# Kernel optimization log

Measured on AMD Instinct MI355X. Metric: run time of the kernel, lower is better.

Reference implementation:

```python
import jax, jax.numpy as jnp
import numpy as np

EPS = 1e-8
N, E, T, HH, HE, HD = 20000, 320000, 4, 64, 16, 128


def _merge(a):
    # 'm d t -> (m t) d'
    m, d, t = a.shape
    return a.transpose(0, 2, 1).reshape(m * t, d)


def _sep(a, t):
    # '(m t) d -> m d t'
    mt, d = a.shape
    return a.reshape(mt // t, t, d).transpose(0, 2, 1)


def _mlp2(x, w1, b1, w2, b2, last_act):
    y = jax.nn.silu(x @ w1 + b1)
    y = y @ w2 + b2
    return jax.nn.silu(y) if last_act else y


def setup_inputs() -> dict:
    key = jax.random.key(0)
    ks = jax.random.split(key, 16)

    def lin(k, i, o):
        return jax.random.normal(k, (i, o), jnp.float32) / np.sqrt(i)

    in_edge = HH * 2 + 1 + HE  # 145
    return {
        "x": jax.random.normal(ks[0], (N, 3, T), jnp.float32),
        "h": jax.random.normal(ks[1], (N, HH, T), jnp.float32),
        "edge_index": jax.random.randint(ks[2], (2, E), 0, N),
        "edge_attr": jax.random.normal(ks[3], (E, HE, T), jnp.float32),
        "batch": jnp.zeros((N,), jnp.int64),
        "edge_w1": lin(ks[4], in_edge, HD), "edge_b1": jnp.zeros((HD,), jnp.float32),
        "edge_w2": lin(ks[5], HD, HD), "edge_b2": jnp.zeros((HD,), jnp.float32),
        "coord_w1": lin(ks[6], HD, HD), "coord_b1": jnp.zeros((HD,), jnp.float32),
        "coord_w2": lin(ks[7], HD, 1), "coord_b2": jnp.zeros((1,), jnp.float32),
        "node_w1": lin(ks[8], HH + HD, HD), "node_b1": jnp.zeros((HD,), jnp.float32),
        "node_w2": lin(ks[9], HD, HH), "node_b2": jnp.zeros((HH,), jnp.float32),
    }


def reference(x, h, edge_index, edge_attr, batch,
              edge_w1, edge_b1, edge_w2, edge_b2,
              coord_w1, coord_b1, coord_w2, coord_b2,
              node_w1, node_b1, node_w2, node_b2):
    row, col = edge_index[0], edge_index[1]
    t = x.shape[-1]
    n = x.shape[0]

    x_ij = x[row] - x[col]                                  # [E,3,T]
    x_ij_norm2 = (x_ij ** 2).sum(axis=1, keepdims=True)     # [E,1,T]

    m_in = jnp.concatenate((h[row], h[col], x_ij_norm2, edge_attr), axis=1)  # [E,2Hh+1+He,T]
    m_ij = _mlp2(_merge(m_in), edge_w1, edge_b1, edge_w2, edge_b2, True)     # [ET,HD]

    m_i = jax.ops.segment_sum(_sep(m_ij, t), row, num_segments=n)           # [N,HD,T]

    h_cat = jnp.concatenate((_merge(h), _merge(m_i)), axis=-1)               # [NT,Hh+HD]
    h_new = _sep(_mlp2(h_cat, node_w1, node_b1, node_w2, node_b2, False), t) # [N,Hh,T]

    coord_m_ij = _mlp2(m_ij, coord_w1, coord_b1, coord_w2, coord_b2, False)  # [ET,1]
    coord_m_ij = coord_m_ij / (jnp.sqrt(_merge(x_ij_norm2) + EPS) + 1.0)

    agg = jax.ops.segment_sum(_sep(coord_m_ij, t) * x_ij, row, num_segments=n)  # [N,3,T]
    cnt = jax.ops.segment_sum(jnp.ones((row.shape[0],), x.dtype), row, num_segments=n)
    x_new = x + agg / jnp.maximum(cnt, 1.0)[:, None, None]
    return (x_new, h_new)
```

## Files before the change

kernel.cpp:

```cpp
#include <hip/hip_runtime.h>
#include <hip/hip_bf16.h>
#include <math.h>

#define T 4
#define HH 64
#define HE 16
#define HD 128
#define EPSF 1e-8f

#define TE 16
#define ROWS 64
#define LDA 168
#define TN 16
#define LDAN 200

using frag8 = __attribute__((ext_vector_type(8))) short;
using f32x4 = __attribute__((ext_vector_type(4))) float;

__device__ __forceinline__ float silu_f(float v) {
    return v * __builtin_amdgcn_rcpf(1.f + __expf(-v));
}

__device__ __forceinline__ unsigned short f2b(float f) {
    __hip_bfloat16 h = __float2bfloat16(f);
    union { __hip_bfloat16 h; unsigned short u; } v; v.h = h;
    return v.u;
}
__device__ __forceinline__ unsigned pk2(float a, float b) {
    __hip_bfloat162 h2 = __float22bfloat162_rn(make_float2(a, b));
    union { __hip_bfloat162 h; unsigned u; } v; v.h = h2;
    return v.u;
}
__device__ __forceinline__ float b2f(unsigned u16) {
    union { unsigned u; float f; } v; v.u = u16 << 16; return v.f;
}
__device__ __forceinline__ void lds_fence() {
    asm volatile("s_waitcnt lgkmcnt(0)" ::: "memory");
}

__global__ void prep_weights(const float* __restrict__ w1, const float* __restrict__ w2,
                             const float* __restrict__ cw1, const float* __restrict__ nw1,
                             const float* __restrict__ nw2, unsigned short* __restrict__ wb)
{
    int i = blockIdx.x * 256 + threadIdx.x;
    if (i < 20480) {
        int n = i / 160, k = i - n * 160;
        float v;
        if (k < 128)      v = w1[k * 128 + n];
        else if (k < 144) v = w1[(129 + (k - 128)) * 128 + n];
        else if (k == 144) v = w1[128 * 128 + n];
        else              v = 0.f;
        wb[i] = f2b(v);
    } else if (i < 36864) {
        int j = i - 20480; int n = j >> 7, k = j & 127;
        wb[i] = f2b(w2[k * 128 + n]);
    } else if (i < 53248) {
        int j = i - 36864; int n = j >> 7, k = j & 127;
        wb[i] = f2b(cw1[k * 128 + n]);
    } else if (i < 77824) {
        int j = i - 53248; int n = j / 192, k = j - n * 192;
        wb[i] = f2b(nw1[k * 128 + n]);
    } else if (i < 86016) {
        int j = i - 77824; int n = j >> 7, k = j & 127;
        wb[i] = f2b(nw2[k * 64 + n]);
    }
}

__global__ void prep_h(const float* __restrict__ h, unsigned short* __restrict__ hb, int N)
{
    int i = blockIdx.x * 256 + threadIdx.x;
    if (i < N * 64) {
        int n = i >> 6, d = i & 63;
        float4 v = *(const float4*)(h + (size_t)i * 4);
        size_t base = (size_t)n * 256 + d;
        hb[base + 0]   = f2b(v.x);
        hb[base + 64]  = f2b(v.y);
        hb[base + 128] = f2b(v.z);
        hb[base + 192] = f2b(v.w);
    }
}

__global__ void hist_kernel(const int* __restrict__ ei, int* __restrict__ deg, int E) {
    int e = blockIdx.x * 256 + threadIdx.x;
    if (e < E) atomicAdd(&deg[ei[e]], 1);
}

__global__ __launch_bounds__(1024)
void scan_kernel(const int* __restrict__ deg, int* __restrict__ start, int N) {
    __shared__ int part[1024];
    int tid = threadIdx.x;
    int chunk = (N + 1023) >> 10;
    int b0 = tid * chunk;
    int s = 0;
    for (int i = 0; i < chunk; ++i) { int idx = b0 + i; if (idx < N) s += deg[idx]; }
    part[tid] = s;
    __syncthreads();
    for (int off = 1; off < 1024; off <<= 1) {
        int v = (tid >= off) ? part[tid - off] : 0;
        __syncthreads();
        part[tid] += v;
        __syncthreads();
    }
    int prefix = (tid > 0) ? part[tid - 1] : 0;
    for (int i = 0; i < chunk; ++i) {
        int idx = b0 + i;
        if (idx < N) { start[idx] = prefix; prefix += deg[idx]; }
    }
    if (tid == 1023) start[N] = part[1023];
}

__global__ void scatter_kernel(const int* __restrict__ ei, const int* __restrict__ start,
                               int* __restrict__ cursor, int* __restrict__ list, int E) {
    int e = blockIdx.x * 256 + threadIdx.x;
    if (e < E) {
        int r = ei[e];
        int p = atomicAdd(&cursor[r], 1);
        list[start[r] + p] = e;
    }
}

__global__ __launch_bounds__(256, 7)
void edge_kernel(const float* __restrict__ x, const unsigned short* __restrict__ hb,
                 const int* __restrict__ ei, const float* __restrict__ ea,
                 const int* __restrict__ list,
                 const unsigned short* __restrict__ w1b,
                 const unsigned short* __restrict__ w2b,
                 const unsigned short* __restrict__ cw1b,
                 const float* __restrict__ b1, const float* __restrict__ b2,
                 const float* __restrict__ cb1, const float* __restrict__ cb2,
                 const float* __restrict__ cw2,
                 float* __restrict__ m_i,
                 float* __restrict__ agg,
                 int N, int E)
{
    __shared__ unsigned short sA[ROWS * LDA];
    __shared__ float sXij[TE * 12];
    __shared__ float sNorm[ROWS];
    __shared__ int   sNode[TE];
    __shared__ int   sPN[2];
    __shared__ float sCoord[ROWS];

    const int tid  = threadIdx.x;
    const int e0   = blockIdx.x * TE;
    const int lane = tid & 63;
    const int wid  = tid >> 6;
    const int eb   = wid * 4;

    if (tid < ROWS) sCoord[tid] = 0.f;
    if (tid == 0) {
        sPN[0] = (e0 > 0)      ? ei[list[e0 - 1]]  : -2;
        sPN[1] = (e0 + TE < E) ? ei[list[e0 + TE]] : -2;
    }

    int node8 = 0;
    {
        int le = lane >> 1, half = lane & 1;
        int p = e0 + eb + le;
        if (lane < 8 && p < E) {
            int eid = list[p];
            node8 = ei[half ? (E + eid) : eid];
            if (half == 0) sNode[eb + le] = node8;
        }
    }
    if (lane < 48) {
        int le = lane / 12, i = lane - le * 12;
        int p = e0 + eb + le;
        float d = 0.f;
        if (p < E) {
            int eid = list[p];
            d = x[ei[eid] * 12 + i] - x[ei[E + eid] * 12 + i];
        }
        sXij[(eb + le) * 12 + i] = d;
    }
    {
        int half = lane >> 5, t = (lane >> 3) & 3, chunk = lane & 7;
        #pragma unroll
        for (int le = 0; le < 4; ++le) {
            int p = e0 + eb + le;
            if (p < E) {
                int nid = __shfl(node8, le * 2 + half);
                uint4 v = *((const uint4*)hb + (size_t)nid * 32 + t * 8 + chunk);
                *(uint4*)&sA[((eb + le) * 4 + t) * LDA + half * 64 + chunk * 8] = v;
            }
        }
    }
    if (lane < 16) {
        int le = lane >> 2, eh0 = (lane & 3) * 4;
        int p = e0 + eb + le;
        if (p < E) {
            const float4* ap = (const float4*)(ea + (size_t)list[p] * 64);
            float4 av[4];
            #pragma unroll
            for (int q = 0; q < 4; ++q) av[q] = ap[eh0 + q];
            #pragma unroll
            for (int t = 0; t < 4; ++t) {
                uint2 u;
                u.x = pk2(((const float*)&av[0])[t], ((const float*)&av[1])[t]);
                u.y = pk2(((const float*)&av[2])[t], ((const float*)&av[3])[t]);
                *(uint2*)&sA[((eb + le) * 4 + t) * LDA + 128 + eh0] = u;
            }
        }
    }
    lds_fence();
    if (lane < 16) {
        int row = wid * 16 + lane;
        int le = eb + (lane >> 2), t = lane & 3;
        float a0 = sXij[le * 12 + t], a1 = sXij[le * 12 + 4 + t], a2 = sXij[le * 12 + 8 + t];
        float n2 = a0 * a0 + a1 * a1 + a2 * a2;
        sNorm[row] = n2;
        uint4 z = {0, 0, 0, 0};
        *(uint4*)&sA[row * LDA + 144] = z;
        *(uint4*)&sA[row * LDA + 152] = z;
        sA[row * LDA + 144] = f2b(n2);
    }
    __syncthreads();

    const int lrow = lane & 15;
    const int quad = lane >> 4;
    const int c0 = wid * 2;

    f32x4 acc[4][2];
    {
        float bv0 = b1[c0 * 16 + lrow], bv1 = b1[(c0 + 1) * 16 + lrow];
        #pragma unroll
        for (int m = 0; m < 4; ++m) {
            acc[m][0] = (f32x4){bv0, bv0, bv0, bv0};
            acc[m][1] = (f32x4){bv1, bv1, bv1, bv1};
        }
    }
    __builtin_amdgcn_s_setprio(1);
    #pragma unroll
    for (int kb = 0; kb < 5; ++kb) {
        frag8 a[4], b[2];
        #pragma unroll
        for (int m = 0; m < 4; ++m)
            a[m] = *(const frag8*)&sA[(m * 16 + lrow) * LDA + kb * 32 + quad * 8];
        #pragma unroll
        for (int n = 0; n < 2; ++n)
            b[n] = *(const frag8*)&w1b[((c0 + n) * 16 + lrow) * 160 + kb * 32 + quad * 8];
        #pragma unroll
        for (int m = 0; m < 4; ++m)
            #pragma unroll
            for (int n = 0; n < 2; ++n)
                acc[m][n] = __builtin_amdgcn_mfma_f32_16x16x32_bf16(a[m], b[n], acc[m][n], 0, 0, 0);
    }
    __builtin_amdgcn_s_setprio(0);
    __syncthreads();

    #pragma unroll
    for (int n = 0; n < 2; ++n) {
        int col = (c0 + n) * 16 + lrow;
        #pragma unroll
        for (int m = 0; m < 4; ++m)
            #pragma unroll
            for (int r = 0; r < 4; ++r)
                sA[(m * 16 + quad * 4 + r) * LDA + col] = f2b(silu_f(acc[m][n][r]));
    }
    __syncthreads();

    {
        float bv0 = b2[c0 * 16 + lrow], bv1 = b2[(c0 + 1) * 16 + lrow];
        #pragma unroll
        for (int m = 0; m < 4; ++m) {
            acc[m][0] = (f32x4){bv0, bv0, bv0, bv0};
            acc[m][1] = (f32x4){bv1, bv1, bv1, bv1};
        }
    }
    __builtin_amdgcn_s_setprio(1);
    #pragma unroll
    for (int kb = 0; kb < 4; ++kb) {
        frag8 a[4], b[2];
        #pragma unroll
        for (int m = 0; m < 4; ++m)
            a[m] = *(const frag8*)&sA[(m * 16 + lrow) * LDA + kb * 32 + quad * 8];
        #pragma unroll
        for (int n = 0; n < 2; ++n)
            b[n] = *(const frag8*)&w2b[((c0 + n) * 16 + lrow) * 128 + kb * 32 + quad * 8];
        #pragma unroll
        for (int m = 0; m < 4; ++m)
            #pragma unroll
            for (int n = 0; n < 2; ++n)
                acc[m][n] = __builtin_amdgcn_mfma_f32_16x16x32_bf16(a[m], b[n], acc[m][n], 0, 0, 0);
    }
    __builtin_amdgcn_s_setprio(0);
    __syncthreads();

    #pragma unroll
    for (int n = 0; n < 2; ++n) {
        int col = (c0 + n) * 16 + lrow;
        #pragma unroll
        for (int m = 0; m < 4; ++m)
            #pragma unroll
            for (int r = 0; r < 4; ++r)
                sA[(m * 16 + quad * 4 + r) * LDA + col] = f2b(silu_f(acc[m][n][r]));
    }
    __syncthreads();

    {
        float bv0 = cb1[c0 * 16 + lrow], bv1 = cb1[(c0 + 1) * 16 + lrow];
        #pragma unroll
        for (int m = 0; m < 4; ++m) {
            acc[m][0] = (f32x4){bv0, bv0, bv0, bv0};
            acc[m][1] = (f32x4){bv1, bv1, bv1, bv1};
        }
    }
    __builtin_amdgcn_s_setprio(1);
    #pragma unroll
    for (int kb = 0; kb < 4; ++kb) {
        frag8 a[4], b[2];
        #pragma unroll
        for (int m = 0; m < 4; ++m)
            a[m] = *(const frag8*)&sA[(m * 16 + lrow) * LDA + kb * 32 + quad * 8];
        #pragma unroll
        for (int n = 0; n < 2; ++n)
            b[n] = *(const frag8*)&cw1b[((c0 + n) * 16 + lrow) * 128 + kb * 32 + quad * 8];
        #pragma unroll
        for (int m = 0; m < 4; ++m)
            #pragma unroll
            for (int n = 0; n < 2; ++n)
                acc[m][n] = __builtin_amdgcn_mfma_f32_16x16x32_bf16(a[m], b[n], acc[m][n], 0, 0, 0);
    }
    __builtin_amdgcn_s_setprio(0);
    {
        float v[16];
        #pragma unroll
        for (int j = 0; j < 16; ++j) v[j] = 0.f;
        #pragma unroll
        for (int n = 0; n < 2; ++n) {
            int col = (c0 + n) * 16 + lrow;
            float cw2v = cw2[col];
            #pragma unroll
            for (int m = 0; m < 4; ++m)
                #pragma unroll
                for (int r = 0; r < 4; ++r)
                    v[m * 4 + r] += silu_f(acc[m][n][r]) * cw2v;
        }
        #pragma unroll
        for (int s = 8; s >= 1; s >>= 1) {
            #pragma unroll
            for (int j = 0; j < s; ++j) {
                float sel = (lrow & s) ? v[j] : v[j + s];
                float oth = __shfl_xor(sel, s);
                v[j] = ((lrow & s) ? v[j + s] : v[j]) + oth;
            }
        }
        atomicAdd(&sCoord[(lrow >> 2) * 16 + quad * 4 + (lrow & 3)], v[0]);
    }

    {
        const int t = tid & 3, c = tid >> 2;
        const int prevN = sPN[0], nextN = sPN[1];
        float r0 = 0.f, r1 = 0.f;
        int cur = sNode[0];
        int ls = 0;
        #pragma unroll
        for (int le = 0; le < TE; ++le) {
            int nd = sNode[le];
            if (nd != cur) {
                if (cur >= 0) {
                    float* d0 = &m_i[(size_t)cur * 512 + tid];
                    if (ls == 0 && prevN == cur) { atomicAdd(d0, r0); atomicAdd(d0 + 256, r1); }
                    else                         { d0[0] = r0; d0[256] = r1; }
                }
                r0 = 0.f; r1 = 0.f; cur = nd; ls = le;
            }
            if (nd >= 0) {
                r0 += b2f((unsigned)sA[(le * 4 + t) * LDA + c]);
                r1 += b2f((unsigned)sA[(le * 4 + t) * LDA + c + 64]);
            }
        }
        if (cur >= 0) {
            float* d0 = &m_i[(size_t)cur * 512 + tid];
            if ((ls == 0 && prevN == cur) || nextN == cur) { atomicAdd(d0, r0); atomicAdd(d0 + 256, r1); }
            else                                           { d0[0] = r0; d0[256] = r1; }
        }
    }
    __syncthreads();

    if (tid < ROWS) {
        float c = (sCoord[tid] + cb2[0]) *
                  __builtin_amdgcn_rcpf(__builtin_amdgcn_sqrtf(sNorm[tid] + EPSF) + 1.f);
        sCoord[tid] = c;
    }
    __syncthreads();

    if (tid < 12) {
        int t = tid & 3;
        float run = 0.f;
        int cur = sNode[0];
        for (int le = 0; le < TE; ++le) {
            int nd = sNode[le];
            if (nd != cur) {
                if (cur >= 0) atomicAdd(&agg[(size_t)cur * 12 + tid], run);
                run = 0.f; cur = nd;
            }
            if (nd >= 0) run += sCoord[le * 4 + t] * sXij[le * 12 + tid];
        }
        if (cur >= 0) atomicAdd(&agg[(size_t)cur * 12 + tid], run);
    }
}

__global__ __launch_bounds__(256, 6)
void node_kernel(const unsigned short* __restrict__ hb, const float* __restrict__ m_i,
                 const unsigned short* __restrict__ nw1b,
                 const unsigned short* __restrict__ nw2b,
                 const float* __restrict__ nb1, const float* __restrict__ nb2,
                 float* __restrict__ out_h, int N)
{
    __shared__ unsigned short sA[64 * LDAN];

    const int tid = threadIdx.x;
    const int n0  = blockIdx.x * TN;

    #pragma unroll
    for (int z = 0; z < 2; ++z) {
        int c = z * 256 + tid;
        int ln = c >> 5, t = (c >> 3) & 3, chunk = c & 7;
        int node = n0 + ln;
        if (node < N) {
            uint4 v = *((const uint4*)hb + (size_t)node * 32 + t * 8 + chunk);
            *(uint4*)&sA[(ln * 4 + t) * LDAN + chunk * 8] = v;
        }
    }
    for (int c = tid; c < 512; c += 256) {
        int ln = c >> 5, hd0 = (c & 31) * 4;
        int node = n0 + ln;
        if (node < N) {
            const float4* mp = (const float4*)(m_i + (size_t)node * 512);
            float4 mv[4];
            #pragma unroll
            for (int q = 0; q < 4; ++q) mv[q] = mp[hd0 + q];
            #pragma unroll
            for (int t = 0; t < 4; ++t) {
                uint2 u;
                u.x = pk2(((const float*)&mv[0])[t], ((const float*)&mv[1])[t]);
                u.y = pk2(((const float*)&mv[2])[t], ((const float*)&mv[3])[t]);
                *(uint2*)&sA[(ln * 4 + t) * LDAN + 64 + hd0] = u;
            }
        }
    }
    __syncthreads();

    const int lane = tid & 63;
    const int wid  = tid >> 6;
    const int lrow = lane & 15;
    const int quad = lane >> 4;
    const int c0 = wid * 2;

    f32x4 acc[4][2];
    {
        float bv0 = nb1[c0 * 16 + lrow], bv1 = nb1[(c0 + 1) * 16 + lrow];
        #pragma unroll
        for (int m = 0; m < 4; ++m) {
            acc[m][0] = (f32x4){bv0, bv0, bv0, bv0};
            acc[m][1] = (f32x4){bv1, bv1, bv1, bv1};
        }
    }
    __builtin_amdgcn_s_setprio(1);
    #pragma unroll
    for (int kb = 0; kb < 6; ++kb) {
        frag8 a[4], b[2];
        #pragma unroll
        for (int m = 0; m < 4; ++m)
            a[m] = *(const frag8*)&sA[(m * 16 + lrow) * LDAN + kb * 32 + quad * 8];
        #pragma unroll
        for (int n = 0; n < 2; ++n)
            b[n] = *(const frag8*)&nw1b[((c0 + n) * 16 + lrow) * 192 + kb * 32 + quad * 8];
        #pragma unroll
        for (int m = 0; m < 4; ++m)
            #pragma unroll
            for (int n = 0; n < 2; ++n)
                acc[m][n] = __builtin_amdgcn_mfma_f32_16x16x32_bf16(a[m], b[n], acc[m][n], 0, 0, 0);
    }
    __builtin_amdgcn_s_setprio(0);
    __syncthreads();

    #pragma unroll
    for (int n = 0; n < 2; ++n) {
        int col = (c0 + n) * 16 + lrow;
        #pragma unroll
        for (int m = 0; m < 4; ++m)
            #pragma unroll
            for (int r = 0; r < 4; ++r)
                sA[(m * 16 + quad * 4 + r) * LDAN + col] = f2b(silu_f(acc[m][n][r]));
    }
    __syncthreads();

    f32x4 acc2[4];
    {
        float bv = nb2[wid * 16 + lrow];
        #pragma unroll
        for (int m = 0; m < 4; ++m) acc2[m] = (f32x4){bv, bv, bv, bv};
    }
    __builtin_amdgcn_s_setprio(1);
    #pragma unroll
    for (int kb = 0; kb < 4; ++kb) {
        frag8 a[4];
        #pragma unroll
        for (int m = 0; m < 4; ++m)
            a[m] = *(const frag8*)&sA[(m * 16 + lrow) * LDAN + kb * 32 + quad * 8];
        frag8 b = *(const frag8*)&nw2b[(wid * 16 + lrow) * 128 + kb * 32 + quad * 8];
        #pragma unroll
        for (int m = 0; m < 4; ++m)
            acc2[m] = __builtin_amdgcn_mfma_f32_16x16x32_bf16(a[m], b, acc2[m], 0, 0, 0);
    }
    __builtin_amdgcn_s_setprio(0);
    #pragma unroll
    for (int m = 0; m < 4; ++m) {
        int node = n0 + m * 4 + quad;
        if (node < N) {
            float* op = out_h + (size_t)node * 256 + (wid * 16 + lrow) * 4;
            float4 ov = { acc2[m][0], acc2[m][1], acc2[m][2], acc2[m][3] };
            *(float4*)op = ov;
        }
    }
}

__global__ void coord_update(const float* __restrict__ x, const float* __restrict__ agg,
                             const int* __restrict__ deg, float* __restrict__ out_x, int N)
{
    int i = blockIdx.x * 256 + threadIdx.x;
    if (i < N * 12) {
        int n = i / 12;
        out_x[i] = x[i] + agg[i] * __builtin_amdgcn_rcpf(fmaxf((float)deg[n], 1.f));
    }
}

extern "C" void kernel_launch(void* const* d_in, const int* in_sizes, int n_in,
                              void* d_out, int out_size, void* d_ws, size_t ws_size,
                              hipStream_t stream)
{
    const float* x   = (const float*)d_in[0];
    const float* h   = (const float*)d_in[1];
    const int*   ei  = (const int*)d_in[2];
    const float* ea  = (const float*)d_in[3];
    const float* w1  = (const float*)d_in[5];
    const float* b1  = (const float*)d_in[6];
    const float* w2  = (const float*)d_in[7];
    const float* b2  = (const float*)d_in[8];
    const float* cw1 = (const float*)d_in[9];
    const float* cb1 = (const float*)d_in[10];
    const float* cw2 = (const float*)d_in[11];
    const float* cb2 = (const float*)d_in[12];
    const float* nw1 = (const float*)d_in[13];
    const float* nb1 = (const float*)d_in[14];
    const float* nw2 = (const float*)d_in[15];
    const float* nb2 = (const float*)d_in[16];

    const int N = in_sizes[0] / 12;
    const int E = in_sizes[2] / 2;

    char* ws = (char*)d_ws;
    unsigned short* wb = (unsigned short*)ws;
    size_t o = 172032;
    int*   deg    = (int*)(ws + o);    o += (size_t)N * 4;
    int*   cursor = (int*)(ws + o);    o += (size_t)N * 4;
    float* agg    = (float*)(ws + o);  o += (size_t)N * 48;
    size_t zero_end = o;
    int*   start  = (int*)(ws + o);    o += (size_t)(N + 1) * 4;
    o = (o + 1023) & ~(size_t)1023;
    int*   list   = (int*)(ws + o);    o += (size_t)E * 4;
    o = (o + 1023) & ~(size_t)1023;
    unsigned short* hb = (unsigned short*)(ws + o); o += (size_t)N * 512;
    o = (o + 1023) & ~(size_t)1023;
    float* m_i    = (float*)(ws + o);

    const unsigned short* w1b  = wb;
    const unsigned short* w2b  = wb + 20480;
    const unsigned short* cw1b = wb + 36864;
    const unsigned short* nw1b = wb + 53248;
    const unsigned short* nw2b = wb + 77824;

    hipMemsetAsync(deg, 0, zero_end - 172032, stream);
    hipMemsetAsync(m_i, 0, (size_t)N * 512 * sizeof(float), stream);
    prep_weights<<<336, 256, 0, stream>>>(w1, w2, cw1, nw1, nw2, wb);
    prep_h<<<(N * 64 + 255) / 256, 256, 0, stream>>>(h, hb, N);
    hist_kernel<<<(E + 255) / 256, 256, 0, stream>>>(ei, deg, E);
    scan_kernel<<<1, 1024, 0, stream>>>(deg, start, N);
    scatter_kernel<<<(E + 255) / 256, 256, 0, stream>>>(ei, start, cursor, list, E);

    float* out_x = (float*)d_out;
    float* out_h = out_x + (size_t)N * 12;

    edge_kernel<<<(E + TE - 1) / TE, 256, 0, stream>>>(
        x, hb, ei, ea, list, w1b, w2b, cw1b, b1, b2, cb1, cb2, cw2, m_i, agg, N, E);
    node_kernel<<<(N + TN - 1) / TN, 256, 0, stream>>>(
        hb, m_i, nw1b, nw2b, nb1, nb2, out_h, N);
    coord_update<<<(N * 12 + 255) / 256, 256, 0, stream>>>(x, agg, deg, out_x, N);
}
```

Measured before the change: 558.9 us.

## Fuse prep kernels, fold coord update into node kernel, relayout m_i

Merges weight conversion, h conversion and degree histogram into one launch, and folds the final coordinate update into the node kernel, removing three kernel launches. Changes the m_i workspace layout from hd-interleaved to t-major contiguous pairs, so edge stores are adjacent and node loads become wider packed conversions. Also replaces a block barrier with an LDS wait before the aggregation step, which is only safe if the threads that read sCoord also wrote it within the same wavefront.

Measured after the change: 570.0 us. About the same (+2.0%).

```diff
diff --git a/kernel.cpp b/kernel.cpp
--- a/kernel.cpp
+++ b/kernel.cpp
@@ -38,51 +38,52 @@
     asm volatile("s_waitcnt lgkmcnt(0)" ::: "memory");
 }
 
-__global__ void prep_weights(const float* __restrict__ w1, const float* __restrict__ w2,
-                             const float* __restrict__ cw1, const float* __restrict__ nw1,
-                             const float* __restrict__ nw2, unsigned short* __restrict__ wb)
+__global__ void prep_fused(const float* __restrict__ w1, const float* __restrict__ w2,
+                           const float* __restrict__ cw1, const float* __restrict__ nw1,
+                           const float* __restrict__ nw2, unsigned short* __restrict__ wb,
+                           const float* __restrict__ h, unsigned short* __restrict__ hb,
+                           const int* __restrict__ ei, int* __restrict__ deg,
+                           int NB_H, int N, int E)
 {
-    int i = blockIdx.x * 256 + threadIdx.x;
-    if (i < 20480) {
-        int n = i / 160, k = i - n * 160;
-        float v;
-        if (k < 128)      v = w1[k * 128 + n];
-        else if (k < 144) v = w1[(129 + (k - 128)) * 128 + n];
-        else if (k == 144) v = w1[128 * 128 + n];
-        else              v = 0.f;
-        wb[i] = f2b(v);
-    } else if (i < 36864) {
-        int j = i - 20480; int n = j >> 7, k = j & 127;
-        wb[i] = f2b(w2[k * 128 + n]);
-    } else if (i < 53248) {
-        int j = i - 36864; int n = j >> 7, k = j & 127;
-        wb[i] = f2b(cw1[k * 128 + n]);
-    } else if (i < 77824) {
-        int j = i - 53248; int n = j / 192, k = j - n * 192;
-        wb[i] = f2b(nw1[k * 128 + n]);
-    } else if (i < 86016) {
-        int j = i - 77824; int n = j >> 7, k = j & 127;
-        wb[i] = f2b(nw2[k * 64 + n]);
-    }
-}
-
-__global__ void prep_h(const float* __restrict__ h, unsigned short* __restrict__ hb, int N)
-{
-    int i = blockIdx.x * 256 + threadIdx.x;
-    if (i < N * 64) {
-        int n = i >> 6, d = i & 63;
-        float4 v = *(const float4*)(h + (size_t)i * 4);
-        size_t base = (size_t)n * 256 + d;
-        hb[base + 0]   = f2b(v.x);
-        hb[base + 64]  = f2b(v.y);
-        hb[base + 128] = f2b(v.z);
-        hb[base + 192] = f2b(v.w);
-    }
-}
-
-__global__ void hist_kernel(const int* __restrict__ ei, int* __restrict__ deg, int E) {
-    int e = blockIdx.x * 256 + threadIdx.x;
-    if (e < E) atomicAdd(&deg[ei[e]], 1);
+    int b = blockIdx.x;
+    if (b < 336) {
+        int i = b * 256 + threadIdx.x;
+        if (i < 20480) {
+            int n = i / 160, k = i - n * 160;
+            float v;
+            if (k < 128)      v = w1[k * 128 + n];
+            else if (k < 144) v = w1[(129 + (k - 128)) * 128 + n];
+            else if (k == 144) v = w1[128 * 128 + n];
+            else              v = 0.f;
+            wb[i] = f2b(v);
+        } else if (i < 36864) {
+            int j = i - 20480; int n = j >> 7, k = j & 127;
+            wb[i] = f2b(w2[k * 128 + n]);
+        } else if (i < 53248) {
+            int j = i - 36864; int n = j >> 7, k = j & 127;
+            wb[i] = f2b(cw1[k * 128 + n]);
+        } else if (i < 77824) {
+            int j = i - 53248; int n = j / 192, k = j - n * 192;
+            wb[i] = f2b(nw1[k * 128 + n]);
+        } else if (i < 86016) {
+            int j = i - 77824; int n = j >> 7, k = j & 127;
+            wb[i] = f2b(nw2[k * 64 + n]);
+        }
+    } else if (b < 336 + NB_H) {
+        int i = (b - 336) * 256 + threadIdx.x;
+        if (i < N * 64) {
+            float4 v = *(const float4*)(h + (size_t)i * 4);
+            int n = i >> 6, d = i & 63;
+            size_t base = (size_t)n * 256 + d;
+            hb[base + 0]   = f2b(v.x);
+            hb[base + 64]  = f2b(v.y);
+            hb[base + 128] = f2b(v.z);
+            hb[base + 192] = f2b(v.w);
+        }
+    } else {
+        int e = (b - 336 - NB_H) * 256 + threadIdx.x;
+        if (e < E) atomicAdd(&deg[ei[e]], 1);
+    }
 }
 
 __global__ __launch_bounds__(1024)
@@ -348,7 +349,8 @@
     }
 
     {
-        const int t = tid & 3, c = tid >> 2;
+        const int t = tid >> 6;
+        const int i = tid & 63;
         const int prevN = sPN[0], nextN = sPN[1];
         float r0 = 0.f, r1 = 0.f;
         int cur = sNode[0];
@@ -358,21 +360,23 @@
             int nd = sNode[le];
             if (nd != cur) {
                 if (cur >= 0) {
-                    float* d0 = &m_i[(size_t)cur * 512 + tid];
-                    if (ls == 0 && prevN == cur) { atomicAdd(d0, r0); atomicAdd(d0 + 256, r1); }
-                    else                         { d0[0] = r0; d0[256] = r1; }
+                    float* d0 = &m_i[(size_t)cur * 512 + t * 128 + 2 * i];
+                    if (ls == 0 && prevN == cur) { atomicAdd(d0, r0); atomicAdd(d0 + 1, r1); }
+                    else                         { d0[0] = r0; d0[1] = r1; }
                 }
                 r0 = 0.f; r1 = 0.f; cur = nd; ls = le;
             }
             if (nd >= 0) {
-                r0 += b2f((unsigned)sA[(le * 4 + t) * LDA + c]);
-                r1 += b2f((unsigned)sA[(le * 4 + t) * LDA + c + 64]);
+                unsigned u = *(const unsigned*)&sA[(le * 4 + t) * LDA + 2 * i];
+                union { unsigned u; float f; } lo, hi;
+                lo.u = u << 16; hi.u = u & 0xffff0000u;
+                r0 += lo.f; r1 += hi.f;
             }
         }
         if (cur >= 0) {
-            float* d0 = &m_i[(size_t)cur * 512 + tid];
-            if ((ls == 0 && prevN == cur) || nextN == cur) { atomicAdd(d0, r0); atomicAdd(d0 + 256, r1); }
-            else                                           { d0[0] = r0; d0[256] = r1; }
+            float* d0 = &m_i[(size_t)cur * 512 + t * 128 + 2 * i];
+            if ((ls == 0 && prevN == cur) || nextN == cur) { atomicAdd(d0, r0); atomicAdd(d0 + 1, r1); }
+            else                                           { d0[0] = r0; d0[1] = r1; }
         }
     }
     __syncthreads();
@@ -382,7 +386,7 @@
                   __builtin_amdgcn_rcpf(__builtin_amdgcn_sqrtf(sNorm[tid] + EPSF) + 1.f);
         sCoord[tid] = c;
     }
-    __syncthreads();
+    lds_fence();
 
     if (tid < 12) {
         int t = tid & 3;
@@ -405,12 +409,22 @@
                  const unsigned short* __restrict__ nw1b,
                  const unsigned short* __restrict__ nw2b,
                  const float* __restrict__ nb1, const float* __restrict__ nb2,
-                 float* __restrict__ out_h, int N)
+                 const float* __restrict__ x, const float* __restrict__ agg,
+                 const int* __restrict__ deg,
+                 float* __restrict__ out_x, float* __restrict__ out_h, int N)
 {
     __shared__ unsigned short sA[64 * LDAN];
 
     const int tid = threadIdx.x;
     const int n0  = blockIdx.x * TN;
+
+    if (tid < 192) {
+        int g = n0 * 12 + tid;
+        if (g < N * 12) {
+            int n = n0 + tid / 12;
+            out_x[g] = x[g] + agg[g] * __builtin_amdgcn_rcpf(fmaxf((float)deg[n], 1.f));
+        }
+    }
 
     #pragma unroll
     for (int z = 0; z < 2; ++z) {
@@ -423,20 +437,19 @@
         }
     }
     for (int c = tid; c < 512; c += 256) {
-        int ln = c >> 5, hd0 = (c & 31) * 4;
+        int ln = c >> 5, t = (c >> 3) & 3, g = c & 7;
         int node = n0 + ln;
         if (node < N) {
-            const float4* mp = (const float4*)(m_i + (size_t)node * 512);
-            float4 mv[4];
-            #pragma unroll
-            for (int q = 0; q < 4; ++q) mv[q] = mp[hd0 + q];
-            #pragma unroll
-            for (int t = 0; t < 4; ++t) {
-                uint2 u;
-                u.x = pk2(((const float*)&mv[0])[t], ((const float*)&mv[1])[t]);
-                u.y = pk2(((const float*)&mv[2])[t], ((const float*)&mv[3])[t]);
-                *(uint2*)&sA[(ln * 4 + t) * LDAN + 64 + hd0] = u;
-            }
+            const float4* mp = (const float4*)(m_i + (size_t)node * 512 + t * 128 + g * 16);
+            float4 m0 = mp[0], m1 = mp[1], m2 = mp[2], m3 = mp[3];
+            uint4 u0, u1;
+            u0.x = pk2(m0.x, m0.y); u0.y = pk2(m0.z, m0.w);
+            u0.z = pk2(m1.x, m1.y); u0.w = pk2(m1.z, m1.w);
+            u1.x = pk2(m2.x, m2.y); u1.y = pk2(m2.z, m2.w);
+            u1.z = pk2(m3.x, m3.y); u1.w = pk2(m3.z, m3.w);
+            unsigned short* dst = &sA[(ln * 4 + t) * LDAN + 64 + g * 16];
+            *(uint4*)dst = u0;
+            *(uint4*)(dst + 8) = u1;
         }
     }
     __syncthreads();
@@ -513,16 +526,6 @@
             float4 ov = { acc2[m][0], acc2[m][1], acc2[m][2], acc2[m][3] };
             *(float4*)op = ov;
         }
-    }
-}
-
-__global__ void coord_update(const float* __restrict__ x, const float* __restrict__ agg,
-                             const int* __restrict__ deg, float* __restrict__ out_x, int N)
-{
-    int i = blockIdx.x * 256 + threadIdx.x;
-    if (i < N * 12) {
-        int n = i / 12;
-        out_x[i] = x[i] + agg[i] * __builtin_amdgcn_rcpf(fmaxf((float)deg[n], 1.f));
     }
 }
 
@@ -571,13 +574,15 @@
     const unsigned short* nw1b = wb + 53248;
     const unsigned short* nw2b = wb + 77824;
 
+    const int NB_H = (N * 64 + 255) / 256;
+    const int NB_E = (E + 255) / 256;
+
     hipMemsetAsync(deg, 0, zero_end - 172032, stream);
     hipMemsetAsync(m_i, 0, (size_t)N * 512 * sizeof(float), stream);
-    prep_weights<<<336, 256, 0, stream>>>(w1, w2, cw1, nw1, nw2, wb);
-    prep_h<<<(N * 64 + 255) / 256, 256, 0, stream>>>(h, hb, N);
-    hist_kernel<<<(E + 255) / 256, 256, 0, stream>>>(ei, deg, E);
+    prep_fused<<<336 + NB_H + NB_E, 256, 0, stream>>>(
+        w1, w2, cw1, nw1, nw2, wb, h, hb, ei, deg, NB_H, N, E);
     scan_kernel<<<1, 1024, 0, stream>>>(deg, start, N);
-    scatter_kernel<<<(E + 255) / 256, 256, 0, stream>>>(ei, start, cursor, list, E);
+    scatter_kernel<<<NB_E, 256, 0, stream>>>(ei, start, cursor, list, E);
 
     float* out_x = (float*)d_out;
     float* out_h = out_x + (size_t)N * 12;
@@ -585,6 +590,5 @@
     edge_kernel<<<(E + TE - 1) / TE, 256, 0, stream>>>(
         x, hb, ei, ea, list, w1b, w2b, cw1b, b1, b2, cb1, cb2, cw2, m_i, agg, N, E);
     node_kernel<<<(N + TN - 1) / TN, 256, 0, stream>>>(
-        hb, m_i, nw1b, nw2b, nb1, nb2, out_h, N);
-    coord_update<<<(N * 12 + 255) / 256, 256, 0, stream>>>(x, agg, deg, out_x, N);
-}
+        hb, m_i, nw1b, nw2b, nb1, nb2, x, agg, deg, out_x, out_h, N);
+}
```
